# Optimization experiments

Measured on AMD Instinct MI355X. Metric: run time of the kernel, lower is better.

## Reference

```python
import jax, jax.numpy as jnp
import numpy as np
from jax import lax


def conv2d(x, w, b, pad):
    y = lax.conv_general_dilated(x, w, (1, 1), [(pad, pad), (pad, pad)],
                                 dimension_numbers=('NCHW', 'OIHW', 'NCHW'))
    return y + b[None, :, None, None]


def grid_sample_bilinear_border(img, grid):
    # img [B,C,H,W], grid [B,h,w,2] normalized to [-1,1] (x,y), align_corners=False
    B, C, H, W = img.shape
    gx, gy = grid[..., 0], grid[..., 1]
    ix = jnp.clip(((gx + 1.0) * W - 1.0) * 0.5, 0.0, W - 1.0)  # border padding = clamp coords
    iy = jnp.clip(((gy + 1.0) * H - 1.0) * 0.5, 0.0, H - 1.0)
    x0f, y0f = jnp.floor(ix), jnp.floor(iy)
    wx, wy = ix - x0f, iy - y0f                       # [B,h,w]
    x0 = jnp.clip(x0f.astype(jnp.int32), 0, W - 1)
    y0 = jnp.clip(y0f.astype(jnp.int32), 0, H - 1)
    x1 = jnp.clip(x0 + 1, 0, W - 1)
    y1 = jnp.clip(y0 + 1, 0, H - 1)
    gather = jax.vmap(lambda im, yi, xi: im[:, yi, xi])  # -> [B,C,h,w]
    v00 = gather(img, y0, x0)
    v01 = gather(img, y0, x1)
    v10 = gather(img, y1, x0)
    v11 = gather(img, y1, x1)
    wx, wy = wx[:, None], wy[:, None]                  # [B,1,h,w]
    return (v00 * (1 - wx) * (1 - wy) + v01 * wx * (1 - wy)
            + v10 * (1 - wx) * wy + v11 * wx * wy)


def setup_inputs():
    key = jax.random.key(0)
    ks = jax.random.split(key, 16)
    B, Ch, H, W = 8, 256, 64, 64
    Cl, h, w = 128, 128, 128
    Co, r = 128, 8
    s = 0.05
    return {
        'f_high': jax.random.normal(ks[0], (B, Ch, H, W), jnp.float32),
        'f_low': jax.random.normal(ks[1], (B, Cl, h, w), jnp.float32),
        'off_w1': jax.random.normal(ks[2], (64, Ch + Cl, 3, 3), jnp.float32) * s,
        'off_b1': jnp.zeros((64,), jnp.float32),
        'off_w2': jax.random.normal(ks[3], (2, 64, 3, 3), jnp.float32) * s,
        'off_b2': jnp.zeros((2,), jnp.float32),
        'proj_w': jax.random.normal(ks[4], (Co, Ch), jnp.float32) * s,
        'proj_b': jnp.zeros((Co,), jnp.float32),
        'ca_w1': jax.random.normal(ks[5], (Co // r, Co), jnp.float32) * s,
        'ca_b1': jnp.zeros((Co // r,), jnp.float32),
        'ca_w2': jax.random.normal(ks[6], (Co, Co // r), jnp.float32) * s,
        'ca_b2': jnp.zeros((Co,), jnp.float32),
        'sa_w': jax.random.normal(ks[7], (1, 2, 7, 7), jnp.float32) * s,
        'sa_b': jnp.zeros((1,), jnp.float32),
    }


def reference(f_high, f_low, off_w1, off_b1, off_w2, off_b2,
              proj_w, proj_b, ca_w1, ca_b1, ca_w2, ca_b2, sa_w, sa_b):
    B, Ch, H, W = f_high.shape
    _, Cl, h, w = f_low.shape
    # resize f_high to (h,w) (bilinear, half-pixel centers == align_corners=False)
    fh_r = jax.image.resize(f_high, (B, Ch, h, w), 'bilinear', antialias=False)
    cat = jnp.concatenate([fh_r, f_low], axis=1)       # [B,Ch+Cl,h,w]
    hid = jax.nn.relu(conv2d(cat, off_w1, off_b1, 1))
    offset = conv2d(hid, off_w2, off_b2, 1)            # [B,2,h,w]
    # base normalized grid (x,y) in [-1,1]
    ys = jnp.linspace(-1.0, 1.0, h, dtype=f_high.dtype)
    xs = jnp.linspace(-1.0, 1.0, w, dtype=f_high.dtype)
    gy, gx = jnp.meshgrid(ys, xs, indexing='ij')
    base = jnp.stack([gx, gy], axis=-1)[None]          # [1,h,w,2]
    scale = jnp.array([2.0 / w, 2.0 / h], dtype=f_high.dtype)
    grid = base + offset.transpose(0, 2, 3, 1) * scale  # [B,h,w,2]
    f_aligned = grid_sample_bilinear_border(f_high, grid)  # [B,Ch,h,w]
    # 1x1 proj Ch -> Co
    x = jnp.einsum('oc,bchw->bohw', proj_w, f_aligned) + proj_b[None, :, None, None]
    # multi-attention fusion: channel (SE) then spatial (CBAM-style)
    p = x.mean(axis=(2, 3))                            # [B,Co]
    a = jax.nn.sigmoid(jax.nn.relu(p @ ca_w1.T + ca_b1) @ ca_w2.T + ca_b2)
    xc = x * a[:, :, None, None]
    sm = jnp.concatenate([xc.mean(axis=1, keepdims=True),
                          xc.max(axis=1, keepdims=True)], axis=1)  # [B,2,h,w]
    sa = jax.nn.sigmoid(conv2d(sm, sa_w, sa_b, 3))
    return xc * sa
```

## Files before the change

### kernel.cpp

```cpp
#include <hip/hip_runtime.h>
#include <hip/hip_fp16.h>
#include <math.h>

typedef _Float16 f16;
typedef _Float16 f16x8 __attribute__((ext_vector_type(8)));
typedef _Float16 f16x2 __attribute__((ext_vector_type(2)));
typedef float f32x4 __attribute__((ext_vector_type(4)));

__global__ __launch_bounds__(256) void pack_conv_w(const float* __restrict__ w,
                                                   f16* __restrict__ out,
                                                   int CIN, int MFR, int COUT) {
  int idx = blockIdx.x * 256 + threadIdx.x;
  int KC = CIN / 32;
  int total = 9 * KC * MFR * 64 * 8;
  if (idx >= total) return;
  int j = idx & 7;
  int lane = (idx >> 3) & 63;
  int rest = idx >> 9;
  int mf = rest % MFR; rest /= MFR;
  int kc = rest % KC; int t = rest / KC;
  int oc = mf * 16 + (lane & 15);
  int c = kc * 32 + (lane >> 4) * 8 + j;
  int ky = t / 3, kx = t % 3;
  float v = (oc < COUT) ? w[((oc * CIN + c) * 3 + ky) * 3 + kx] : 0.f;
  out[idx] = (f16)v;
}

__global__ __launch_bounds__(256) void pack_proj_w(const float* __restrict__ w,
                                                   f16* __restrict__ out) {
  int idx = blockIdx.x * 256 + threadIdx.x;
  int j = idx & 7; int lane = (idx >> 3) & 63; int rest = idx >> 9;
  int mf = rest & 7; int kc = rest >> 3;
  int oc = mf * 16 + (lane & 15);
  int c = kc * 32 + (lane >> 4) * 8 + j;
  out[idx] = (f16)w[oc * 256 + c];
}

__global__ __launch_bounds__(256) void k_fhw(const float* __restrict__ fh,
                                             f16* __restrict__ fhw) {
  __shared__ float lds[128 * 17];
  int wg = blockIdx.x;
  int xt = wg & 3; int ch2 = (wg >> 2) & 1; int y = (wg >> 3) & 63; int b = wg >> 9;
  int x0 = xt * 16;
  int tid = threadIdx.x;
  for (int i = 0; i < 8; ++i) {
    int u = i * 256 + tid;
    int c = u >> 4, xi = u & 15;
    lds[c * 17 + xi] = fh[(((size_t)b * 256 + ch2 * 128 + c) * 64 + y) * 64 + x0 + xi];
  }
  __syncthreads();
  {
    int x = tid >> 4, cl = tid & 15;
    f16x8 v;
    #pragma unroll
    for (int j = 0; j < 8; ++j) v[j] = (f16)lds[(cl * 8 + j) * 17 + x];
    int coct = ch2 * 16 + cl;
    *(f16x8*)&fhw[(((size_t)b * 64 + y) * 64 + x0 + x) * 256 + coct * 8] = v;
  }
}

__global__ __launch_bounds__(256) void k_catA(const f16* __restrict__ fhw,
                                              f16* __restrict__ cat) {
  int wg = blockIdx.x;
  int Y = wg & 127, b = wg >> 7;
  float iy = fminf(fmaxf(Y * 0.5f - 0.25f, 0.f), 63.f);
  int y0 = (int)iy; float wy = iy - y0; int y1 = min(y0 + 1, 63);
  int tid = threadIdx.x;
  for (int i = 0; i < 16; ++i) {
    int u = i * 256 + tid; int X = u >> 5, coct = u & 31;
    float ix = fminf(fmaxf(X * 0.5f - 0.25f, 0.f), 63.f);
    int x0 = (int)ix; float wx = ix - x0; int x1 = min(x0 + 1, 63);
    f16x8 v00 = *(const f16x8*)&fhw[(((size_t)b * 64 + y0) * 64 + x0) * 256 + coct * 8];
    f16x8 v01 = *(const f16x8*)&fhw[(((size_t)b * 64 + y0) * 64 + x1) * 256 + coct * 8];
    f16x8 v10 = *(const f16x8*)&fhw[(((size_t)b * 64 + y1) * 64 + x0) * 256 + coct * 8];
    f16x8 v11 = *(const f16x8*)&fhw[(((size_t)b * 64 + y1) * 64 + x1) * 256 + coct * 8];
    f16x8 r;
    #pragma unroll
    for (int j = 0; j < 8; ++j) {
      float t0 = (1.f - wx) * (float)v00[j] + wx * (float)v01[j];
      float t1 = (1.f - wx) * (float)v10[j] + wx * (float)v11[j];
      r[j] = (f16)((1.f - wy) * t0 + wy * t1);
    }
    *(f16x8*)&cat[((size_t)b * 16384 + Y * 128 + X) * 384 + coct * 8] = r;
  }
}

__global__ __launch_bounds__(256) void k_catB(const float* __restrict__ fl,
                                              f16* __restrict__ cat) {
  __shared__ float lds[128 * 17];
  int wg = blockIdx.x;
  int xt = wg & 7; int Y = (wg >> 3) & 127; int b = wg >> 10;
  int x0 = xt * 16; int tid = threadIdx.x;
  for (int i = 0; i < 8; ++i) {
    int u = i * 256 + tid; int c = u >> 4, xi = u & 15;
    lds[c * 17 + xi] = fl[(((size_t)b * 128 + c) * 128 + Y) * 128 + x0 + xi];
  }
  __syncthreads();
  {
    int x = tid >> 4, coct = tid & 15;
    f16x8 v;
    #pragma unroll
    for (int j = 0; j < 8; ++j) v[j] = (f16)lds[(coct * 8 + j) * 17 + x];
    *(f16x8*)&cat[((size_t)b * 16384 + Y * 128 + x0 + x) * 384 + 256 + coct * 8] = v;
  }
}

template<int CIN, int MFR, int COUT, bool RELU>
__global__ __launch_bounds__(256) void k_conv3(const f16* __restrict__ in,
                                               const f16* __restrict__ apack,
                                               const float* __restrict__ bias,
                                               f16* __restrict__ out) {
  constexpr int KC = CIN / 32;
  constexpr int LDSH = 18 * 18 * 32;
  constexpr int LDSO = 256 * COUT;
  constexpr int LDSN = LDSH > LDSO ? LDSH : LDSO;
  __shared__ f16 lds[LDSN];
  char* ldsb = (char*)lds;
  int wg = blockIdx.x;
  int tx = wg & 7, ty = (wg >> 3) & 7, b = wg >> 6;
  int y0 = ty * 16, x0 = tx * 16;
  int tid = threadIdx.x; int lane = tid & 63; int w = tid >> 6;
  f32x4 acc[MFR][4];
  #pragma unroll
  for (int m = 0; m < MFR; ++m)
    #pragma unroll
    for (int n = 0; n < 4; ++n) acc[m][n] = (f32x4){0.f, 0.f, 0.f, 0.f};

  for (int kc = 0; kc < KC; ++kc) {
    __syncthreads();
    for (int u = tid; u < 18 * 18 * 4; u += 256) {
      int coct = u & 3; int p = u >> 2; int px = p % 18, py = p / 18;
      int gy = y0 + py - 1, gx = x0 + px - 1;
      f16x8 v = {0, 0, 0, 0, 0, 0, 0, 0};
      if (gy >= 0 && gy < 128 && gx >= 0 && gx < 128)
        v = *(const f16x8*)&in[(((size_t)b * 128 + gy) * 128 + gx) * CIN + kc * 32 + coct * 8];
      int addr = (((py * 18 + px) * 64) + coct * 16) ^ (((px >> 1) & 3) << 4);
      *(f16x8*)(ldsb + addr) = v;
    }
    __syncthreads();
    #pragma unroll
    for (int t = 0; t < 9; ++t) {
      int ky = t / 3, kx = t % 3;
      f16x8 af[MFR];
      #pragma unroll
      for (int m = 0; m < MFR; ++m)
        af[m] = *(const f16x8*)&apack[(size_t)(((t * KC + kc) * MFR + m) * 64 + lane) * 8];
      #pragma unroll
      for (int n = 0; n < 4; ++n) {
        int py = w * 4 + n + ky;
        int px = (lane & 15) + kx;
        int addr = ((py * 18 + px) * 64 + ((lane >> 4) * 16)) ^ (((px >> 1) & 3) << 4);
        f16x8 bf = *(const f16x8*)(ldsb + addr);
        #pragma unroll
        for (int m = 0; m < MFR; ++m)
          acc[m][n] = __builtin_amdgcn_mfma_f32_16x16x32_f16(af[m], bf, acc[m][n], 0, 0, 0);
      }
    }
  }
  __syncthreads();
  #pragma unroll
  for (int m = 0; m < MFR; ++m)
    #pragma unroll
    for (int n = 0; n < 4; ++n) {
      int pos = w * 64 + n * 16 + (lane & 15);
      #pragma unroll
      for (int rp = 0; rp < 2; ++rp) {
        int ch = m * 16 + (lane >> 4) * 4 + rp * 2;
        if (ch < COUT) {
          float v0 = acc[m][n][rp * 2 + 0] + bias[ch];
          float v1 = acc[m][n][rp * 2 + 1] + bias[ch + 1];
          if (RELU) { v0 = fmaxf(v0, 0.f); v1 = fmaxf(v1, 0.f); }
          f16x2 pk; pk[0] = (f16)v0; pk[1] = (f16)v1;
          int addr = ((pos * COUT + ch) * 2) ^ ((pos & 7) << 4);
          *(f16x2*)(ldsb + addr) = pk;
        }
      }
    }
  __syncthreads();
  for (int u = tid; u < 256 * COUT / 2; u += 256) {
    int pos = u / (COUT / 2); int cp = u % (COUT / 2);
    int addr = ((pos * COUT + cp * 2) * 2) ^ ((pos & 7) << 4);
    f16x2 v = *(const f16x2*)(ldsb + addr);
    int y = y0 + (pos >> 4), x = x0 + (pos & 15);
    *(f16x2*)&out[(((size_t)b * 128 + y) * 128 + x) * COUT + cp * 2] = v;
  }
}

__global__ __launch_bounds__(256) void k_gp(const f16* __restrict__ fhw,
                                            const f16* __restrict__ off,
                                            const f16* __restrict__ ppack,
                                            const float* __restrict__ pbias,
                                            float* __restrict__ x,
                                            float* __restrict__ psum) {
  __shared__ f16 bt[64 * 256];
  __shared__ float4 samp[64];
  char* ldsb = (char*)bt;
  int wg = blockIdx.x;
  int b = wg & 7, tile = wg >> 3;
  int pbase = tile * 64;
  int tid = threadIdx.x, lane = tid & 63, w = tid >> 6;
  if (tid < 64) {
    int pos = pbase + tid;
    int yy = pos >> 7, xx = pos & 127;
    float o0 = (float)off[((size_t)b * 16384 + pos) * 2 + 0];
    float o1 = (float)off[((size_t)b * 16384 + pos) * 2 + 1];
    float gx = -1.f + xx * (2.f / 127.f) + o0 * (1.f / 64.f);
    float gy = -1.f + yy * (2.f / 127.f) + o1 * (1.f / 64.f);
    float ix = fminf(fmaxf((gx + 1.f) * 32.f - 0.5f, 0.f), 63.f);
    float iy = fminf(fmaxf((gy + 1.f) * 32.f - 0.5f, 0.f), 63.f);
    float x0f = floorf(ix), y0f = floorf(iy);
    samp[tid] = make_float4(x0f, y0f, ix - x0f, iy - y0f);
  }
  __syncthreads();
  for (int i = 0; i < 8; ++i) {
    int u = i * 256 + tid; int p = u >> 5, coct = u & 31;
    float4 s = samp[p];
    int x0i = (int)s.x, y0i = (int)s.y;
    int x1i = min(x0i + 1, 63), y1i = min(y0i + 1, 63);
    float wx = s.z, wy = s.w;
    const f16* bb = fhw + (size_t)b * 4096 * 256 + coct * 8;
    f16x8 v00 = *(const f16x8*)&bb[(y0i * 64 + x0i) * 256];
    f16x8 v01 = *(const f16x8*)&bb[(y0i * 64 + x1i) * 256];
    f16x8 v10 = *(const f16x8*)&bb[(y1i * 64 + x0i) * 256];
    f16x8 v11 = *(const f16x8*)&bb[(y1i * 64 + x1i) * 256];
    f16x8 r;
    #pragma unroll
    for (int j = 0; j < 8; ++j) {
      float t0 = (1.f - wx) * (float)v00[j] + wx * (float)v01[j];
      float t1 = (1.f - wx) * (float)v10[j] + wx * (float)v11[j];
      r[j] = (f16)((1.f - wy) * t0 + wy * t1);
    }
    int addr = (p * 512 + coct * 16) ^ ((p & 7) << 4);
    *(f16x8*)(ldsb + addr) = r;
  }
  __syncthreads();
  f32x4 acc[2][4];
  #pragma unroll
  for (int m = 0; m < 2; ++m)
    #pragma unroll
    for (int n = 0; n < 4; ++n) acc[m][n] = (f32x4){0.f, 0.f, 0.f, 0.f};
  #pragma unroll
  for (int kc = 0; kc < 8; ++kc) {
    f16x8 af[2];
    #pragma unroll
    for (int m = 0; m < 2; ++m)
      af[m] = *(const f16x8*)&ppack[(size_t)((kc * 8 + w * 2 + m) * 64 + lane) * 8];
    #pragma unroll
    for (int n = 0; n < 4; ++n) {
      int p = n * 16 + (lane & 15);
      int addr = (p * 512 + kc * 64 + ((lane >> 4) * 16)) ^ ((p & 7) << 4);
      f16x8 bf = *(const f16x8*)(ldsb + addr);
      #pragma unroll
      for (int m = 0; m < 2; ++m)
        acc[m][n] = __builtin_amdgcn_mfma_f32_16x16x32_f16(af[m], bf, acc[m][n], 0, 0, 0);
    }
  }
  __syncthreads();
  #pragma unroll
  for (int m = 0; m < 2; ++m)
    #pragma unroll
    for (int n = 0; n < 4; ++n) {
      int p = n * 16 + (lane & 15);
      #pragma unroll
      for (int r = 0; r < 4; ++r) {
        int ch = w * 32 + m * 16 + (lane >> 4) * 4 + r;
        int addr = ((p * 128 + ch) * 4) ^ ((p & 7) << 4);
        *(float*)(ldsb + addr) = acc[m][n][r];
      }
    }
  __syncthreads();
  float part = 0.f;
  int c = tid & 127;
  float bc = pbias[c];
  for (int i = 0; i < 32; ++i) {
    int u = i * 256 + tid; int p = u >> 7;
    float v = *(const float*)(ldsb + (((p * 128 + c) * 4) ^ ((p & 7) << 4))) + bc;
    x[((size_t)b * 16384 + pbase + p) * 128 + c] = v;
    part += v;
  }
  __syncthreads();
  float* rl = (float*)ldsb;
  rl[tid] = part;
  __syncthreads();
  if (tid < 128) psum[(size_t)wg * 128 + tid] = rl[tid] + rl[tid + 128];
}

__global__ __launch_bounds__(128) void k_ca(const float* __restrict__ psum,
                                            const float* __restrict__ w1, const float* __restrict__ b1,
                                            const float* __restrict__ w2, const float* __restrict__ b2,
                                            float* __restrict__ a) {
  __shared__ float pl[128];
  __shared__ float hl[16];
  int b = blockIdx.x; int tid = threadIdx.x;
  float s = 0.f;
  for (int t = 0; t < 256; ++t) s += psum[(size_t)(t * 8 + b) * 128 + tid];
  pl[tid] = s * (1.f / 16384.f);
  __syncthreads();
  if (tid < 16) {
    float h = b1[tid];
    for (int c = 0; c < 128; ++c) h += pl[c] * w1[tid * 128 + c];
    hl[tid] = fmaxf(h, 0.f);
  }
  __syncthreads();
  float z = b2[tid];
  #pragma unroll
  for (int o2 = 0; o2 < 16; ++o2) z += hl[o2] * w2[tid * 16 + o2];
  a[b * 128 + tid] = 1.f / (1.f + expf(-z));
}

__global__ __launch_bounds__(256) void k_sm(const float* __restrict__ x,
                                            const float* __restrict__ a,
                                            float* __restrict__ meanp, float* __restrict__ maxp) {
  __shared__ float al[128];
  int wg = blockIdx.x;
  int pbase = wg * 128;
  int b = pbase >> 14;
  int tid = threadIdx.x;
  if (tid < 128) al[tid] = a[b * 128 + tid];
  __syncthreads();
  for (int i = 0; i < 16; ++i) {
    int u = i * 256 + tid;
    int p = u >> 5, q = u & 31;
    float4 v = *(const float4*)&x[((size_t)pbase + p) * 128 + q * 4];
    float sm = 0.f, mx = -1e30f;
    float vv[4] = {v.x, v.y, v.z, v.w};
    #pragma unroll
    for (int j = 0; j < 4; ++j) {
      float xc = vv[j] * al[q * 4 + j];
      sm += xc; mx = fmaxf(mx, xc);
    }
    #pragma unroll
    for (int d = 1; d < 32; d <<= 1) {
      sm += __shfl_xor(sm, d);
      mx = fmaxf(mx, __shfl_xor(mx, d));
    }
    if ((tid & 31) == 0) {
      meanp[pbase + p] = sm * (1.f / 128.f);
      maxp[pbase + p] = mx;
    }
  }
}

__global__ __launch_bounds__(256) void k_sa(const float* __restrict__ meanp,
                                            const float* __restrict__ maxp,
                                            const float* __restrict__ sw, const float* __restrict__ sb,
                                            float* __restrict__ sap) {
  __shared__ float lds[2][22][22];
  __shared__ float wl[98];
  int wg = blockIdx.x;
  int tx = wg & 7, ty = (wg >> 3) & 7, b = wg >> 6;
  int y0 = ty * 16, x0 = tx * 16;
  int tid = threadIdx.x;
  if (tid < 98) wl[tid] = sw[tid];
  for (int u = tid; u < 2 * 22 * 22; u += 256) {
    int ch = u / 484; int p = u % 484; int py = p / 22, px = p % 22;
    int gy = y0 + py - 3, gx = x0 + px - 3;
    float v = 0.f;
    if (gy >= 0 && gy < 128 && gx >= 0 && gx < 128)
      v = ch ? maxp[(size_t)b * 16384 + gy * 128 + gx] : meanp[(size_t)b * 16384 + gy * 128 + gx];
    lds[ch][py][px] = v;
  }
  __syncthreads();
  int py = tid >> 4, px = tid & 15;
  float accv = sb[0];
  #pragma unroll
  for (int ch = 0; ch < 2; ++ch)
    for (int ky = 0; ky < 7; ++ky)
      #pragma unroll
      for (int kx = 0; kx < 7; ++kx)
        accv += lds[ch][py + ky][px + kx] * wl[ch * 49 + ky * 7 + kx];
  sap[(size_t)b * 16384 + (y0 + py) * 128 + x0 + px] = 1.f / (1.f + expf(-accv));
}

__global__ __launch_bounds__(256) void k_out(const float* __restrict__ x,
                                             const float* __restrict__ a,
                                             const float* __restrict__ sap,
                                             float* __restrict__ out) {
  __shared__ float lds[32 * 129];
  __shared__ float al[128];
  __shared__ float sl[32];
  int wg = blockIdx.x;
  int pbase = wg * 32; int b = pbase >> 14;
  int tid = threadIdx.x;
  if (tid < 128) al[tid] = a[b * 128 + tid];
  if (tid < 32) sl[tid] = sap[pbase + tid];
  __syncthreads();
  for (int i = 0; i < 4; ++i) {
    int u = i * 256 + tid;
    int p = u >> 5, q = u & 31;
    float4 v = *(const float4*)&x[((size_t)pbase + p) * 128 + q * 4];
    lds[p * 129 + q * 4 + 0] = v.x;
    lds[p * 129 + q * 4 + 1] = v.y;
    lds[p * 129 + q * 4 + 2] = v.z;
    lds[p * 129 + q * 4 + 3] = v.w;
  }
  __syncthreads();
  for (int i = 0; i < 16; ++i) {
    int u = i * 256 + tid; int c = u >> 5, p = u & 31;
    float v = lds[p * 129 + c] * al[c] * sl[p];
    out[((size_t)(b * 128 + c)) * 16384 + (pbase & 16383) + p] = v;
  }
}

extern "C" void kernel_launch(void* const* d_in, const int* in_sizes, int n_in,
                              void* d_out, int out_size, void* d_ws, size_t ws_size,
                              hipStream_t stream) {
  const float* f_high = (const float*)d_in[0];
  const float* f_low  = (const float*)d_in[1];
  const float* off_w1 = (const float*)d_in[2];
  const float* off_b1 = (const float*)d_in[3];
  const float* off_w2 = (const float*)d_in[4];
  const float* off_b2 = (const float*)d_in[5];
  const float* proj_w = (const float*)d_in[6];
  const float* proj_b = (const float*)d_in[7];
  const float* ca_w1  = (const float*)d_in[8];
  const float* ca_b1  = (const float*)d_in[9];
  const float* ca_w2  = (const float*)d_in[10];
  const float* ca_b2  = (const float*)d_in[11];
  const float* sa_w   = (const float*)d_in[12];
  const float* sa_b   = (const float*)d_in[13];
  float* out = (float*)d_out;

  char* ws = (char*)d_ws; size_t o = 0;
  auto alloc = [&](size_t b) { char* p = ws + o; o += (b + 255) & ~(size_t)255; return p; };
  f16*   fhw  = (f16*)alloc(8ull * 4096 * 256 * 2);
  f16*   cat  = (f16*)alloc(8ull * 16384 * 384 * 2);
  f16*   hid  = (f16*)alloc(8ull * 16384 * 64 * 2);
  f16*   offb = (f16*)alloc(8ull * 16384 * 2 * 2);
  f16*   ap1  = (f16*)alloc(221184ull * 2);
  f16*   ap2  = (f16*)alloc(9216ull * 2);
  f16*   pp   = (f16*)alloc(32768ull * 2);
  float* xbuf = (float*)alloc(8ull * 16384 * 128 * 4);
  float* ps   = (float*)alloc(2048ull * 128 * 4);
  float* av   = (float*)alloc(8ull * 128 * 4);
  float* mp   = (float*)alloc(131072ull * 4);
  float* xp   = (float*)alloc(131072ull * 4);
  float* sp   = (float*)alloc(131072ull * 4);

  pack_conv_w<<<864, 256, 0, stream>>>(off_w1, ap1, 384, 4, 64);
  pack_conv_w<<<36, 256, 0, stream>>>(off_w2, ap2, 64, 1, 2);
  pack_proj_w<<<128, 256, 0, stream>>>(proj_w, pp);
  k_fhw<<<4096, 256, 0, stream>>>(f_high, fhw);
  k_catA<<<1024, 256, 0, stream>>>(fhw, cat);
  k_catB<<<8192, 256, 0, stream>>>(f_low, cat);
  k_conv3<384, 4, 64, true><<<512, 256, 0, stream>>>(cat, ap1, off_b1, hid);
  k_conv3<64, 1, 2, false><<<512, 256, 0, stream>>>(hid, ap2, off_b2, offb);
  k_gp<<<2048, 256, 0, stream>>>(fhw, offb, pp, proj_b, xbuf, ps);
  k_ca<<<8, 128, 0, stream>>>(ps, ca_w1, ca_b1, ca_w2, ca_b2, av);
  k_sm<<<1024, 256, 0, stream>>>(xbuf, av, mp, xp);
  k_sa<<<512, 256, 0, stream>>>(mp, xp, sa_w, sa_b, sp);
  k_out<<<4096, 256, 0, stream>>>(xbuf, av, sp, out);
}
```

Measured before the change: 378.2 us.

## Double-buffer conv input via global_load_lds with padded layout; store proj output in fp16

The cat and hid buffers get a zero border (130x130), filled once by a new zero kernel. This lets the 3x3 conv stage its input patch with unconditional global_load_lds into double-buffered LDS, overlapping the next channel chunk's load with the current MFMAs. The conv inner loop is reordered so each B fragment loaded from LDS is reused across the three ky taps, and it runs under raised wave priority. The projected activation x is stored as fp16 instead of fp32, roughly halving traffic in k_gp, k_sm and k_out. The cost is extra workspace, an added kernel launch and some precision loss in x.

```diff
diff --git a/kernel.cpp b/kernel.cpp
--- a/kernel.cpp
+++ b/kernel.cpp
@@ -6,6 +6,11 @@
 typedef _Float16 f16x8 __attribute__((ext_vector_type(8)));
 typedef _Float16 f16x2 __attribute__((ext_vector_type(2)));
 typedef float f32x4 __attribute__((ext_vector_type(4)));
+
+__device__ __forceinline__ void gll16(const void* g, void* l) {
+  __builtin_amdgcn_global_load_lds((const __attribute__((address_space(1))) void*)g,
+                                   (__attribute__((address_space(3))) void*)l, 16, 0, 0);
+}
 
 __global__ __launch_bounds__(256) void pack_conv_w(const float* __restrict__ w,
                                                    f16* __restrict__ out,
@@ -36,6 +41,27 @@
   out[idx] = (f16)w[oc * 256 + c];
 }
 
+__global__ __launch_bounds__(256) void k_zero(f16* __restrict__ cat, f16* __restrict__ hid) {
+  int idx = blockIdx.x * 256 + threadIdx.x;
+  f16x8 z = {(f16)0, (f16)0, (f16)0, (f16)0, (f16)0, (f16)0, (f16)0, (f16)0};
+  int p, b, c8;
+  f16* dst; int C;
+  if (idx < 198144) {
+    c8 = idx % 48; int rest = idx / 48; p = rest % 516; b = rest / 516;
+    dst = cat; C = 384;
+  } else {
+    int i2 = idx - 198144;
+    c8 = i2 % 8; int rest = i2 / 8; p = rest % 516; b = rest / 516;
+    dst = hid; C = 64;
+  }
+  int y, x;
+  if (p < 130) { y = 0; x = p; }
+  else if (p < 260) { y = 129; x = p - 130; }
+  else if (p < 388) { y = p - 260 + 1; x = 0; }
+  else { y = p - 388 + 1; x = 129; }
+  *(f16x8*)&dst[(((size_t)b * 130 + y) * 130 + x) * C + c8 * 8] = z;
+}
+
 __global__ __launch_bounds__(256) void k_fhw(const float* __restrict__ fh,
                                              f16* __restrict__ fhw) {
   __shared__ float lds[128 * 17];
@@ -81,7 +107,7 @@
       float t1 = (1.f - wx) * (float)v10[j] + wx * (float)v11[j];
       r[j] = (f16)((1.f - wy) * t0 + wy * t1);
     }
-    *(f16x8*)&cat[((size_t)b * 16384 + Y * 128 + X) * 384 + coct * 8] = r;
+    *(f16x8*)&cat[(((size_t)b * 130 + 1 + Y) * 130 + 1 + X) * 384 + coct * 8] = r;
   }
 }
 
@@ -101,71 +127,93 @@
     f16x8 v;
     #pragma unroll
     for (int j = 0; j < 8; ++j) v[j] = (f16)lds[(coct * 8 + j) * 17 + x];
-    *(f16x8*)&cat[((size_t)b * 16384 + Y * 128 + x0 + x) * 384 + 256 + coct * 8] = v;
-  }
-}
-
-template<int CIN, int MFR, int COUT, bool RELU>
-__global__ __launch_bounds__(256) void k_conv3(const f16* __restrict__ in,
-                                               const f16* __restrict__ apack,
-                                               const float* __restrict__ bias,
-                                               f16* __restrict__ out) {
+    *(f16x8*)&cat[(((size_t)b * 130 + 1 + Y) * 130 + 1 + x0 + x) * 384 + 256 + coct * 8] = v;
+  }
+}
+
+template<int CIN, int MFR, int COUT, bool RELU, int OPAD>
+__global__ __launch_bounds__(256, 2) void k_conv3(const f16* __restrict__ in,
+                                                  const f16* __restrict__ apack,
+                                                  const float* __restrict__ bias,
+                                                  f16* __restrict__ out) {
   constexpr int KC = CIN / 32;
-  constexpr int LDSH = 18 * 18 * 32;
-  constexpr int LDSO = 256 * COUT;
-  constexpr int LDSN = LDSH > LDSO ? LDSH : LDSO;
-  __shared__ f16 lds[LDSN];
-  char* ldsb = (char*)lds;
+  constexpr int PATCH = 21504;
+  __shared__ __align__(16) char ldsb[2 * PATCH];
   int wg = blockIdx.x;
   int tx = wg & 7, ty = (wg >> 3) & 7, b = wg >> 6;
   int y0 = ty * 16, x0 = tx * 16;
-  int tid = threadIdx.x; int lane = tid & 63; int w = tid >> 6;
+  int tid = threadIdx.x, lane = tid & 63, w = tid >> 6;
+  int lx = lane & 15, hi = lane >> 4, w4 = w * 4;
+
+  int ro[6];
+  #pragma unroll
+  for (int j = 0; j < 6; ++j) {
+    int s = j * 256 + w * 64 + lane;
+    if (s > 1295) s = 1295;
+    int p = s >> 2, coct = s & 3;
+    int py = p / 18, px = p % 18;
+    int cocts = coct ^ ((px >> 1) & 3);
+    ro[j] = ((y0 + py) * 130 + (x0 + px)) * CIN + cocts * 8;
+  }
+  const f16* inb = in + (size_t)b * 130 * 130 * CIN;
+
   f32x4 acc[MFR][4];
   #pragma unroll
   for (int m = 0; m < MFR; ++m)
     #pragma unroll
     for (int n = 0; n < 4; ++n) acc[m][n] = (f32x4){0.f, 0.f, 0.f, 0.f};
 
+  auto stage = [&](int kc, int buf) {
+    #pragma unroll
+    for (int j = 0; j < 6; ++j) {
+      if (j < 5 || w == 0) {
+        gll16(inb + ro[j] + kc * 32, ldsb + buf * PATCH + (j * 256 + w * 64) * 16);
+      }
+    }
+  };
+
+  stage(0, 0);
+  __syncthreads();
   for (int kc = 0; kc < KC; ++kc) {
-    __syncthreads();
-    for (int u = tid; u < 18 * 18 * 4; u += 256) {
-      int coct = u & 3; int p = u >> 2; int px = p % 18, py = p / 18;
-      int gy = y0 + py - 1, gx = x0 + px - 1;
-      f16x8 v = {0, 0, 0, 0, 0, 0, 0, 0};
-      if (gy >= 0 && gy < 128 && gx >= 0 && gx < 128)
-        v = *(const f16x8*)&in[(((size_t)b * 128 + gy) * 128 + gx) * CIN + kc * 32 + coct * 8];
-      int addr = (((py * 18 + px) * 64) + coct * 16) ^ (((px >> 1) & 3) << 4);
-      *(f16x8*)(ldsb + addr) = v;
-    }
-    __syncthreads();
-    #pragma unroll
-    for (int t = 0; t < 9; ++t) {
-      int ky = t / 3, kx = t % 3;
-      f16x8 af[MFR];
+    if (kc + 1 < KC) stage(kc + 1, (kc + 1) & 1);
+    const char* cb = ldsb + (kc & 1) * PATCH;
+    __builtin_amdgcn_s_setprio(1);
+    #pragma unroll
+    for (int kx = 0; kx < 3; ++kx) {
+      int px = lx + kx;
+      int sw = (px >> 1) & 3;
+      f16x8 bf[6];
       #pragma unroll
-      for (int m = 0; m < MFR; ++m)
-        af[m] = *(const f16x8*)&apack[(size_t)(((t * KC + kc) * MFR + m) * 64 + lane) * 8];
+      for (int s = 0; s < 6; ++s) {
+        int slot = ((w4 + s) * 18 + px) * 4 + (hi ^ sw);
+        bf[s] = *(const f16x8*)(cb + slot * 16);
+      }
       #pragma unroll
-      for (int n = 0; n < 4; ++n) {
-        int py = w * 4 + n + ky;
-        int px = (lane & 15) + kx;
-        int addr = ((py * 18 + px) * 64 + ((lane >> 4) * 16)) ^ (((px >> 1) & 3) << 4);
-        f16x8 bf = *(const f16x8*)(ldsb + addr);
+      for (int ky = 0; ky < 3; ++ky) {
+        f16x8 af[MFR];
         #pragma unroll
         for (int m = 0; m < MFR; ++m)
-          acc[m][n] = __builtin_amdgcn_mfma_f32_16x16x32_f16(af[m], bf, acc[m][n], 0, 0, 0);
+          af[m] = *(const f16x8*)&apack[(size_t)((((ky * 3 + kx) * KC + kc) * MFR + m) * 64 + lane) * 8];
+        #pragma unroll
+        for (int n = 0; n < 4; ++n)
+          #pragma unroll
+          for (int m = 0; m < MFR; ++m)
+            acc[m][n] = __builtin_amdgcn_mfma_f32_16x16x32_f16(af[m], bf[n + ky], acc[m][n], 0, 0, 0);
       }
     }
-  }
-  __syncthreads();
+    __builtin_amdgcn_s_setprio(0);
+    __syncthreads();
+  }
+
+  constexpr int S = 128 + 2 * OPAD;
   #pragma unroll
   for (int m = 0; m < MFR; ++m)
     #pragma unroll
     for (int n = 0; n < 4; ++n) {
-      int pos = w * 64 + n * 16 + (lane & 15);
+      int pos = w * 64 + n * 16 + lx;
       #pragma unroll
       for (int rp = 0; rp < 2; ++rp) {
-        int ch = m * 16 + (lane >> 4) * 4 + rp * 2;
+        int ch = m * 16 + hi * 4 + rp * 2;
         if (ch < COUT) {
           float v0 = acc[m][n][rp * 2 + 0] + bias[ch];
           float v1 = acc[m][n][rp * 2 + 1] + bias[ch + 1];
@@ -181,8 +229,8 @@
     int pos = u / (COUT / 2); int cp = u % (COUT / 2);
     int addr = ((pos * COUT + cp * 2) * 2) ^ ((pos & 7) << 4);
     f16x2 v = *(const f16x2*)(ldsb + addr);
-    int y = y0 + (pos >> 4), x = x0 + (pos & 15);
-    *(f16x2*)&out[(((size_t)b * 128 + y) * 128 + x) * COUT + cp * 2] = v;
+    int y = y0 + (pos >> 4) + OPAD, x = x0 + (pos & 15) + OPAD;
+    *(f16x2*)&out[(((size_t)b * S + y) * S + x) * COUT + cp * 2] = v;
   }
 }
 
@@ -190,7 +238,7 @@
                                             const f16* __restrict__ off,
                                             const f16* __restrict__ ppack,
                                             const float* __restrict__ pbias,
-                                            float* __restrict__ x,
+                                            f16* __restrict__ x,
                                             float* __restrict__ psum) {
   __shared__ f16 bt[64 * 256];
   __shared__ float4 samp[64];
@@ -269,20 +317,26 @@
       }
     }
   __syncthreads();
-  float part = 0.f;
-  int c = tid & 127;
-  float bc = pbias[c];
-  for (int i = 0; i < 32; ++i) {
-    int u = i * 256 + tid; int p = u >> 7;
-    float v = *(const float*)(ldsb + (((p * 128 + c) * 4) ^ ((p & 7) << 4))) + bc;
-    x[((size_t)b * 16384 + pbase + p) * 128 + c] = v;
-    part += v;
+  float part0 = 0.f, part1 = 0.f;
+  int cp = tid & 63, wv = tid >> 6;
+  int c0 = cp * 2;
+  float b0 = pbias[c0], b1 = pbias[c0 + 1];
+  #pragma unroll
+  for (int i = 0; i < 16; ++i) {
+    int p = i * 4 + wv;
+    float v0 = *(const float*)(ldsb + (((p * 128 + c0) * 4) ^ ((p & 7) << 4)));
+    float v1 = *(const float*)(ldsb + (((p * 128 + c0 + 1) * 4) ^ ((p & 7) << 4)));
+    v0 += b0; v1 += b1;
+    f16x2 pk; pk[0] = (f16)v0; pk[1] = (f16)v1;
+    *(f16x2*)&x[((size_t)b * 16384 + pbase + p) * 128 + c0] = pk;
+    part0 += v0; part1 += v1;
   }
   __syncthreads();
   float* rl = (float*)ldsb;
-  rl[tid] = part;
-  __syncthreads();
-  if (tid < 128) psum[(size_t)wg * 128 + tid] = rl[tid] + rl[tid + 128];
+  rl[wv * 128 + c0] = part0; rl[wv * 128 + c0 + 1] = part1;
+  __syncthreads();
+  if (tid < 128)
+    psum[(size_t)wg * 128 + tid] = rl[tid] + rl[128 + tid] + rl[256 + tid] + rl[384 + tid];
 }
 
 __global__ __launch_bounds__(128) void k_ca(const float* __restrict__ psum,
@@ -308,7 +362,7 @@
   a[b * 128 + tid] = 1.f / (1.f + expf(-z));
 }
 
-__global__ __launch_bounds__(256) void k_sm(const float* __restrict__ x,
+__global__ __launch_bounds__(256) void k_sm(const f16* __restrict__ x,
                                             const float* __restrict__ a,
                                             float* __restrict__ meanp, float* __restrict__ maxp) {
   __shared__ float al[128];
@@ -318,23 +372,23 @@
   int tid = threadIdx.x;
   if (tid < 128) al[tid] = a[b * 128 + tid];
   __syncthreads();
-  for (int i = 0; i < 16; ++i) {
+  #pragma unroll
+  for (int i = 0; i < 8; ++i) {
     int u = i * 256 + tid;
-    int p = u >> 5, q = u & 31;
-    float4 v = *(const float4*)&x[((size_t)pbase + p) * 128 + q * 4];
+    int p = u >> 4, q = u & 15;
+    f16x8 v = *(const f16x8*)&x[((size_t)pbase + p) * 128 + q * 8];
     float sm = 0.f, mx = -1e30f;
-    float vv[4] = {v.x, v.y, v.z, v.w};
-    #pragma unroll
-    for (int j = 0; j < 4; ++j) {
-      float xc = vv[j] * al[q * 4 + j];
+    #pragma unroll
+    for (int j = 0; j < 8; ++j) {
+      float xc = (float)v[j] * al[q * 8 + j];
       sm += xc; mx = fmaxf(mx, xc);
     }
     #pragma unroll
-    for (int d = 1; d < 32; d <<= 1) {
+    for (int d = 1; d < 16; d <<= 1) {
       sm += __shfl_xor(sm, d);
       mx = fmaxf(mx, __shfl_xor(mx, d));
     }
-    if ((tid & 31) == 0) {
+    if ((tid & 15) == 0) {
       meanp[pbase + p] = sm * (1.f / 128.f);
       maxp[pbase + p] = mx;
     }
@@ -372,7 +426,7 @@
   sap[(size_t)b * 16384 + (y0 + py) * 128 + x0 + px] = 1.f / (1.f + expf(-accv));
 }
 
-__global__ __launch_bounds__(256) void k_out(const float* __restrict__ x,
+__global__ __launch_bounds__(256) void k_out(const f16* __restrict__ x,
                                              const float* __restrict__ a,
                                              const float* __restrict__ sap,
                                              float* __restrict__ out) {
@@ -385,16 +439,16 @@
   if (tid < 128) al[tid] = a[b * 128 + tid];
   if (tid < 32) sl[tid] = sap[pbase + tid];
   __syncthreads();
-  for (int i = 0; i < 4; ++i) {
+  #pragma unroll
+  for (int i = 0; i < 2; ++i) {
     int u = i * 256 + tid;
-    int p = u >> 5, q = u & 31;
-    float4 v = *(const float4*)&x[((size_t)pbase + p) * 128 + q * 4];
-    lds[p * 129 + q * 4 + 0] = v.x;
-    lds[p * 129 + q * 4 + 1] = v.y;
-    lds[p * 129 + q * 4 + 2] = v.z;
-    lds[p * 129 + q * 4 + 3] = v.w;
-  }
-  __syncthreads();
+    int p = u >> 4, q = u & 15;
+    f16x8 v = *(const f16x8*)&x[((size_t)pbase + p) * 128 + q * 8];
+    #pragma unroll
+    for (int j = 0; j < 8; ++j) lds[p * 129 + q * 8 + j] = (float)v[j];
+  }
+  __syncthreads();
+  #pragma unroll
   for (int i = 0; i < 16; ++i) {
     int u = i * 256 + tid; int c = u >> 5, p = u & 31;
     float v = lds[p * 129 + c] * al[c] * sl[p];
@@ -424,13 +478,13 @@
   char* ws = (char*)d_ws; size_t o = 0;
   auto alloc = [&](size_t b) { char* p = ws + o; o += (b + 255) & ~(size_t)255; return p; };
   f16*   fhw  = (f16*)alloc(8ull * 4096 * 256 * 2);
-  f16*   cat  = (f16*)alloc(8ull * 16384 * 384 * 2);
-  f16*   hid  = (f16*)alloc(8ull * 16384 * 64 * 2);
+  f16*   cat  = (f16*)alloc(8ull * 130 * 130 * 384 * 2);
+  f16*   hid  = (f16*)alloc(8ull * 130 * 130 * 64 * 2);
   f16*   offb = (f16*)alloc(8ull * 16384 * 2 * 2);
   f16*   ap1  = (f16*)alloc(221184ull * 2);
   f16*   ap2  = (f16*)alloc(9216ull * 2);
   f16*   pp   = (f16*)alloc(32768ull * 2);
-  float* xbuf = (float*)alloc(8ull * 16384 * 128 * 4);
+  f16*   xbuf = (f16*)alloc(8ull * 16384 * 128 * 2);
   float* ps   = (float*)alloc(2048ull * 128 * 4);
   float* av   = (float*)alloc(8ull * 128 * 4);
   float* mp   = (float*)alloc(131072ull * 4);
@@ -440,11 +494,12 @@
   pack_conv_w<<<864, 256, 0, stream>>>(off_w1, ap1, 384, 4, 64);
   pack_conv_w<<<36, 256, 0, stream>>>(off_w2, ap2, 64, 1, 2);
   pack_proj_w<<<128, 256, 0, stream>>>(proj_w, pp);
+  k_zero<<<903, 256, 0, stream>>>(cat, hid);
   k_fhw<<<4096, 256, 0, stream>>>(f_high, fhw);
   k_catA<<<1024, 256, 0, stream>>>(fhw, cat);
   k_catB<<<8192, 256, 0, stream>>>(f_low, cat);
-  k_conv3<384, 4, 64, true><<<512, 256, 0, stream>>>(cat, ap1, off_b1, hid);
-  k_conv3<64, 1, 2, false><<<512, 256, 0, stream>>>(hid, ap2, off_b2, offb);
+  k_conv3<384, 4, 64, true, 1><<<512, 256, 0, stream>>>(cat, ap1, off_b1, hid);
+  k_conv3<64, 1, 2, false, 0><<<512, 256, 0, stream>>>(hid, ap2, off_b2, offb);
   k_gp<<<2048, 256, 0, stream>>>(fhw, offb, pp, proj_b, xbuf, ps);
   k_ca<<<8, 128, 0, stream>>>(ps, ca_w1, ca_b1, ca_w2, ca_b2, av);
   k_sm<<<1024, 256, 0, stream>>>(xbuf, av, mp, xp);
```

New measurement: 342.0 us. -9.6%, faster.
